# Kernel tuning notes

Hardware: AMD Instinct MI355X
Metric: run time of the kernel (lower is better)

The kernel has to match this reference:

```python
import jax, jax.numpy as jnp
import numpy as np

B, N, M = 2, 16384, 16
D_IN, D_MODEL, D_OUT = 64, 128, 128


def _gather(x, idx):
    # x: (B, N, C), idx: (B, N, M) -> (B, N, M, C)
    return jax.vmap(lambda a, i: a[i])(x, idx)


def setup_inputs() -> dict:
    key = jax.random.key(0)
    ks = jax.random.split(key, 20)

    def w(k, shape, fan_in):
        return (jax.random.normal(k, shape, jnp.float32) / np.sqrt(fan_in)).astype(jnp.float32)

    return {
        "xyz": jax.random.normal(ks[0], (B, N, 3), jnp.float32),
        "feature": jax.random.normal(ks[1], (B, N, D_IN), jnp.float32),
        "neighbors_idx": jax.random.randint(ks[2], (B, N, M), 0, N, jnp.int32),
        # fc_delta: Linear(3, d_model) -> ReLU -> Linear(d_model, d_model)
        "delta_w1": w(ks[3], (3, D_MODEL), 3), "delta_b1": jnp.zeros((D_MODEL,), jnp.float32),
        "delta_w2": w(ks[4], (D_MODEL, D_MODEL), D_MODEL), "delta_b2": jnp.zeros((D_MODEL,), jnp.float32),
        # fc1: Linear(d_in, d_model)
        "fc1_w": w(ks[5], (D_IN, D_MODEL), D_IN), "fc1_b": jnp.zeros((D_MODEL,), jnp.float32),
        # w_qs/w_ks/w_vs: Linear(d_model, d_model, bias=False)
        "wq": w(ks[6], (D_MODEL, D_MODEL), D_MODEL),
        "wk": w(ks[7], (D_MODEL, D_MODEL), D_MODEL),
        "wv": w(ks[8], (D_MODEL, D_MODEL), D_MODEL),
        # fc_gamma: Linear -> ReLU -> Linear
        "gamma_w1": w(ks[9], (D_MODEL, D_MODEL), D_MODEL), "gamma_b1": jnp.zeros((D_MODEL,), jnp.float32),
        "gamma_w2": w(ks[10], (D_MODEL, D_MODEL), D_MODEL), "gamma_b2": jnp.zeros((D_MODEL,), jnp.float32),
        # fc2: Linear(d_model, d_out)
        "fc2_w": w(ks[11], (D_MODEL, D_OUT), D_MODEL), "fc2_b": jnp.zeros((D_OUT,), jnp.float32),
        # shortcut_fc: Linear(d_in, d_out)
        "sc_w": w(ks[12], (D_IN, D_OUT), D_IN), "sc_b": jnp.zeros((D_OUT,), jnp.float32),
    }


def reference(xyz, feature, neighbors_idx,
              delta_w1, delta_b1, delta_w2, delta_b2,
              fc1_w, fc1_b, wq, wk, wv,
              gamma_w1, gamma_b1, gamma_w2, gamma_b2,
              fc2_w, fc2_b, sc_w, sc_b):
    # relative positions of k neighbors: (B, N, M, 3)
    raw = xyz[:, :, None, :] - _gather(xyz, neighbors_idx)
    # fc1 projection
    f = feature @ fc1_w + fc1_b                       # (B, N, Dm)
    knn_f = _gather(f, neighbors_idx)                 # (B, N, M, Dm)
    q = f @ wq                                        # (B, N, Dm)
    k = knn_f @ wk                                    # (B, N, M, Dm)
    v = knn_f @ wv                                    # (B, N, M, Dm)
    # positional MLP
    pos = jax.nn.relu(raw @ delta_w1 + delta_b1) @ delta_w2 + delta_b2
    # vector attention scores per channel
    attn = q[:, :, None, :] - k + pos
    attn = jax.nn.relu(attn @ gamma_w1 + gamma_b1) @ gamma_w2 + gamma_b2
    attn = jax.nn.softmax(attn / np.sqrt(D_MODEL), axis=-2)  # softmax over M
    # weighted sum over neighbors
    out = jnp.einsum('bnmf,bnmf->bnf', attn, v + pos)  # (B, N, Dm)
    out = out @ fc2_w + fc2_b + (feature @ sc_w + sc_b)
    return out
```

## Files before the change

kernel.cpp:

```cpp
#include <hip/hip_runtime.h>

#define BATCH 2
#define NPTS  16384
#define BN    (BATCH * NPTS)
#define DIN   64
#define DM    128
#define NM    16

__global__ __launch_bounds__(256) void k_proj(
    const float* __restrict__ feat,
    const float* __restrict__ fc1_w, const float* __restrict__ fc1_b,
    const float* __restrict__ wq, const float* __restrict__ wk, const float* __restrict__ wv,
    const float* __restrict__ sc_w, const float* __restrict__ sc_b,
    float* __restrict__ qo, float* __restrict__ kfo, float* __restrict__ vfo,
    float* __restrict__ outp)
{
    __shared__ __align__(16) float featb[64][DIN];
    __shared__ __align__(16) float fbuf[64][DM];
    const int tid = threadIdx.x;
    const int p0  = blockIdx.x * 64;

    #pragma unroll
    for (int k = 0; k < 4; ++k) {
        int i4 = tid + k * 256;
        ((float4*)featb)[i4] = ((const float4*)(feat + (size_t)p0 * DIN))[i4];
    }
    __syncthreads();

    const int j    = tid & 127;
    const int base = (tid >> 7) * 32;
    float acc[32];

    #pragma unroll
    for (int pp = 0; pp < 32; ++pp) acc[pp] = fc1_b[j];
    for (int c = 0; c < DIN; c += 4) {
        float w0 = fc1_w[(c + 0) * DM + j];
        float w1 = fc1_w[(c + 1) * DM + j];
        float w2 = fc1_w[(c + 2) * DM + j];
        float w3 = fc1_w[(c + 3) * DM + j];
        #pragma unroll
        for (int pp = 0; pp < 32; ++pp) {
            float4 a = *(const float4*)&featb[base + pp][c];
            acc[pp] += a.x * w0 + a.y * w1 + a.z * w2 + a.w * w3;
        }
    }
    #pragma unroll
    for (int pp = 0; pp < 32; ++pp) fbuf[base + pp][j] = acc[pp];
    __syncthreads();

    for (int pass = 0; pass < 3; ++pass) {
        const float* W = pass == 0 ? wq : (pass == 1 ? wk : wv);
        float*       O = pass == 0 ? qo : (pass == 1 ? kfo : vfo);
        #pragma unroll
        for (int pp = 0; pp < 32; ++pp) acc[pp] = 0.f;
        for (int c = 0; c < DM; c += 4) {
            float w0 = W[(c + 0) * DM + j];
            float w1 = W[(c + 1) * DM + j];
            float w2 = W[(c + 2) * DM + j];
            float w3 = W[(c + 3) * DM + j];
            #pragma unroll
            for (int pp = 0; pp < 32; ++pp) {
                float4 a = *(const float4*)&fbuf[base + pp][c];
                acc[pp] += a.x * w0 + a.y * w1 + a.z * w2 + a.w * w3;
            }
        }
        #pragma unroll
        for (int pp = 0; pp < 32; ++pp) O[(size_t)(p0 + base + pp) * DM + j] = acc[pp];
    }

    #pragma unroll
    for (int pp = 0; pp < 32; ++pp) acc[pp] = sc_b[j];
    for (int c = 0; c < DIN; c += 4) {
        float w0 = sc_w[(c + 0) * DM + j];
        float w1 = sc_w[(c + 1) * DM + j];
        float w2 = sc_w[(c + 2) * DM + j];
        float w3 = sc_w[(c + 3) * DM + j];
        #pragma unroll
        for (int pp = 0; pp < 32; ++pp) {
            float4 a = *(const float4*)&featb[base + pp][c];
            acc[pp] += a.x * w0 + a.y * w1 + a.z * w2 + a.w * w3;
        }
    }
    #pragma unroll
    for (int pp = 0; pp < 32; ++pp) outp[(size_t)(p0 + base + pp) * DM + j] = acc[pp];
}

#define ASW(r) (((r) >> 1) & 3)

#define FMA16(O, W) do { \
    O[0]  += a0.x * (W); O[1]  += a0.y * (W); O[2]  += a0.z * (W); O[3]  += a0.w * (W); \
    O[4]  += a1.x * (W); O[5]  += a1.y * (W); O[6]  += a1.z * (W); O[7]  += a1.w * (W); \
    O[8]  += a2.x * (W); O[9]  += a2.y * (W); O[10] += a2.z * (W); O[11] += a2.w * (W); \
    O[12] += a3.x * (W); O[13] += a3.y * (W); O[14] += a3.z * (W); O[15] += a3.w * (W); } while (0)

__device__ __forceinline__ void mm128(
    const float* __restrict__ Wg,
    float (* __restrict__ wbuf)[DM],
    const float (* __restrict__ aw)[NM],
    float* __restrict__ o0, float* __restrict__ o1,
    int tid, int lane)
{
    for (int c0 = 0; c0 < DM; c0 += 16) {
        __syncthreads();
        #pragma unroll
        for (int k2 = 0; k2 < 2; ++k2) {
            int i4 = tid + k2 * 256;
            ((float4*)wbuf)[i4] = ((const float4*)(Wg + (size_t)c0 * DM))[i4];
        }
        __syncthreads();
        #pragma unroll
        for (int cc = 0; cc < 16; ++cc) {
            const int s = (cc >> 1) & 3;
            float w0 = wbuf[cc][lane];
            float w1 = wbuf[cc][64 + lane];
            const float4* ar = (const float4*)&aw[c0 + cc][0];
            const float4 a0 = ar[0 ^ s];
            const float4 a1 = ar[1 ^ s];
            const float4 a2 = ar[2 ^ s];
            const float4 a3 = ar[3 ^ s];
            FMA16(o0, w0);
            FMA16(o1, w1);
        }
    }
}

__global__ __launch_bounds__(256, 2) void k_attn(
    const float* __restrict__ xyz, const int* __restrict__ nidx,
    const float* __restrict__ qg, const float* __restrict__ kfg, const float* __restrict__ vfg,
    const float* __restrict__ dw1, const float* __restrict__ db1,
    const float* __restrict__ dw2, const float* __restrict__ db2,
    const float* __restrict__ gw1, const float* __restrict__ gb1,
    const float* __restrict__ gw2, const float* __restrict__ gb2,
    float* __restrict__ ao)
{
    __shared__ __align__(16) float abuf[4][DM][NM];
    __shared__ __align__(16) float obuf[4][NM][DM];
    __shared__ __align__(16) float wbuf[16][DM];
    __shared__ __align__(16) float raws[4][NM][4];
    __shared__ int idxs[4][NM];

    const int tid  = threadIdx.x;
    const int wave = tid >> 6;
    const int lane = tid & 63;
    const int p    = blockIdx.x * 4 + wave;
    const int b    = p >> 14;

    if (lane < NM) {
        int jj = nidx[(size_t)p * NM + lane];
        idxs[wave][lane] = jj;
        const float* xc = xyz + (size_t)p * 3;
        const float* xn = xyz + ((size_t)b * NPTS + jj) * 3;
        raws[wave][lane][0] = xc[0] - xn[0];
        raws[wave][lane][1] = xc[1] - xn[1];
        raws[wave][lane][2] = xc[2] - xn[2];
        raws[wave][lane][3] = 0.f;
    }
    const float q0 = qg[(size_t)p * DM + lane];
    const float q1 = qg[(size_t)p * DM + 64 + lane];
    __syncthreads();

    const int sw = ASW(lane);
    float4* arow0 = (float4*)&abuf[wave][lane][0];
    float4* arow1 = (float4*)&abuf[wave][64 + lane][0];

    #pragma unroll 4
    for (int m = 0; m < NM; ++m) {
        int jj = idxs[wave][m];
        size_t r = ((size_t)b * NPTS + jj) * DM;
        obuf[wave][m][lane]      = q0 - kfg[r + lane];
        obuf[wave][m][64 + lane] = q1 - kfg[r + 64 + lane];
    }

    float o0[16], o1[16];

    {
        float wA0 = dw1[lane],          wB0 = dw1[64 + lane];
        float wA1 = dw1[DM + lane],     wB1 = dw1[DM + 64 + lane];
        float wA2 = dw1[2 * DM + lane], wB2 = dw1[2 * DM + 64 + lane];
        float bA = db1[lane], bB = db1[64 + lane];
        #pragma unroll
        for (int m = 0; m < NM; ++m) {
            float4 r4 = *(const float4*)&raws[wave][m][0];
            o0[m] = fmaxf(bA + r4.x * wA0 + r4.y * wA1 + r4.z * wA2, 0.f);
            o1[m] = fmaxf(bB + r4.x * wB0 + r4.y * wB1 + r4.z * wB2, 0.f);
        }
        #pragma unroll
        for (int g = 0; g < 4; ++g) {
            arow0[g ^ sw] = make_float4(o0[4*g+0], o0[4*g+1], o0[4*g+2], o0[4*g+3]);
            arow1[g ^ sw] = make_float4(o1[4*g+0], o1[4*g+1], o1[4*g+2], o1[4*g+3]);
        }
    }

    {
        float bA = db2[lane], bB = db2[64 + lane];
        #pragma unroll
        for (int m = 0; m < NM; ++m) { o0[m] = bA; o1[m] = bB; }
    }
    mm128(dw2, wbuf, abuf[wave], o0, o1, tid, lane);

    #pragma unroll
    for (int g = 0; g < 4; ++g) {
        float4 t0, t1;
        t0.x = obuf[wave][4*g+0][lane] + o0[4*g+0];
        t0.y = obuf[wave][4*g+1][lane] + o0[4*g+1];
        t0.z = obuf[wave][4*g+2][lane] + o0[4*g+2];
        t0.w = obuf[wave][4*g+3][lane] + o0[4*g+3];
        t1.x = obuf[wave][4*g+0][64 + lane] + o1[4*g+0];
        t1.y = obuf[wave][4*g+1][64 + lane] + o1[4*g+1];
        t1.z = obuf[wave][4*g+2][64 + lane] + o1[4*g+2];
        t1.w = obuf[wave][4*g+3][64 + lane] + o1[4*g+3];
        arow0[g ^ sw] = t0;
        arow1[g ^ sw] = t1;
    }
    #pragma unroll 4
    for (int m = 0; m < NM; ++m) {
        int jj = idxs[wave][m];
        size_t r = ((size_t)b * NPTS + jj) * DM;
        obuf[wave][m][lane]      = vfg[r + lane] + o0[m];
        obuf[wave][m][64 + lane] = vfg[r + 64 + lane] + o1[m];
    }

    {
        float bA = gb1[lane], bB = gb1[64 + lane];
        #pragma unroll
        for (int m = 0; m < NM; ++m) { o0[m] = bA; o1[m] = bB; }
    }
    mm128(gw1, wbuf, abuf[wave], o0, o1, tid, lane);
    #pragma unroll
    for (int g = 0; g < 4; ++g) {
        arow0[g ^ sw] = make_float4(fmaxf(o0[4*g+0], 0.f), fmaxf(o0[4*g+1], 0.f),
                                    fmaxf(o0[4*g+2], 0.f), fmaxf(o0[4*g+3], 0.f));
        arow1[g ^ sw] = make_float4(fmaxf(o1[4*g+0], 0.f), fmaxf(o1[4*g+1], 0.f),
                                    fmaxf(o1[4*g+2], 0.f), fmaxf(o1[4*g+3], 0.f));
    }

    {
        float bA = gb2[lane], bB = gb2[64 + lane];
        #pragma unroll
        for (int m = 0; m < NM; ++m) { o0[m] = bA; o1[m] = bB; }
    }
    mm128(gw2, wbuf, abuf[wave], o0, o1, tid, lane);

    const float scale = 0.08838834764831845f;
    float mx0 = -1e30f, mx1 = -1e30f;
    #pragma unroll
    for (int m = 0; m < NM; ++m) {
        o0[m] *= scale; o1[m] *= scale;
        mx0 = fmaxf(mx0, o0[m]); mx1 = fmaxf(mx1, o1[m]);
    }
    float s0 = 0.f, s1 = 0.f, r0 = 0.f, r1 = 0.f;
    #pragma unroll
    for (int m = 0; m < NM; ++m) {
        float e0 = __expf(o0[m] - mx0);
        float e1 = __expf(o1[m] - mx1);
        s0 += e0; s1 += e1;
        r0 += e0 * obuf[wave][m][lane];
        r1 += e1 * obuf[wave][m][64 + lane];
    }
    ao[(size_t)p * DM + lane]      = r0 / s0;
    ao[(size_t)p * DM + 64 + lane] = r1 / s1;
}

__global__ __launch_bounds__(256) void k_final(
    const float* __restrict__ aog,
    const float* __restrict__ fc2_w, const float* __restrict__ fc2_b,
    float* __restrict__ outp)
{
    __shared__ __align__(16) float ab[64][DM];
    const int tid = threadIdx.x;
    const int p0  = blockIdx.x * 64;

    #pragma unroll
    for (int k = 0; k < 8; ++k) {
        int i4 = tid + k * 256;
        ((float4*)ab)[i4] = ((const float4*)(aog + (size_t)p0 * DM))[i4];
    }
    __syncthreads();

    const int j    = tid & 127;
    const int base = (tid >> 7) * 32;
    float acc[32];
    #pragma unroll
    for (int pp = 0; pp < 32; ++pp) acc[pp] = fc2_b[j];
    for (int c = 0; c < DM; c += 4) {
        float w0 = fc2_w[(c + 0) * DM + j];
        float w1 = fc2_w[(c + 1) * DM + j];
        float w2 = fc2_w[(c + 2) * DM + j];
        float w3 = fc2_w[(c + 3) * DM + j];
        #pragma unroll
        for (int pp = 0; pp < 32; ++pp) {
            float4 a = *(const float4*)&ab[base + pp][c];
            acc[pp] += a.x * w0 + a.y * w1 + a.z * w2 + a.w * w3;
        }
    }
    #pragma unroll
    for (int pp = 0; pp < 32; ++pp) {
        size_t o = (size_t)(p0 + base + pp) * DM + j;
        outp[o] += acc[pp];
    }
}

extern "C" void kernel_launch(void* const* d_in, const int* in_sizes, int n_in,
                              void* d_out, int out_size, void* d_ws, size_t ws_size,
                              hipStream_t stream)
{
    const float* xyz     = (const float*)d_in[0];
    const float* feature = (const float*)d_in[1];
    const int*   nidx    = (const int*)d_in[2];
    const float* dw1     = (const float*)d_in[3];
    const float* db1     = (const float*)d_in[4];
    const float* dw2     = (const float*)d_in[5];
    const float* db2     = (const float*)d_in[6];
    const float* fc1_w   = (const float*)d_in[7];
    const float* fc1_b   = (const float*)d_in[8];
    const float* wq      = (const float*)d_in[9];
    const float* wk      = (const float*)d_in[10];
    const float* wv      = (const float*)d_in[11];
    const float* gw1     = (const float*)d_in[12];
    const float* gb1     = (const float*)d_in[13];
    const float* gw2     = (const float*)d_in[14];
    const float* gb2     = (const float*)d_in[15];
    const float* fc2_w   = (const float*)d_in[16];
    const float* fc2_b   = (const float*)d_in[17];
    const float* sc_w    = (const float*)d_in[18];
    const float* sc_b    = (const float*)d_in[19];

    float* ws = (float*)d_ws;
    const size_t SZ = (size_t)BN * DM;
    float* q  = ws;
    float* kf = ws + SZ;
    float* vf = ws + 2 * SZ;
    float* ao = q;
    float* out = (float*)d_out;

    k_proj<<<BN / 64, 256, 0, stream>>>(feature, fc1_w, fc1_b, wq, wk, wv,
                                        sc_w, sc_b, q, kf, vf, out);
    k_attn<<<BN / 4, 256, 0, stream>>>(xyz, nidx, q, kf, vf,
                                       dw1, db1, dw2, db2,
                                       gw1, gb1, gw2, gb2, ao);
    k_final<<<BN / 64, 256, 0, stream>>>(ao, fc2_w, fc2_b, out);
}
```

Before: 1.140 ms.

## Keep gathered K/V in registers and read weights directly from global

The attention kernel drops the shared obuf, wbuf, raws and idxs buffers and every __syncthreads. Neighbor indices, gathered K and V rows, and relative positions are now loaded straight into per-lane registers. Weight rows are read from global or L2 inside the matmul loop instead of being staged cooperatively in shared memory. This removes block-wide barriers and shared traffic, so each wave runs independently. The cost is 64 extra live registers per lane, which may cut occupancy under launch_bounds(256,2), plus repeated global weight loads per wave.

```diff
diff --git a/kernel.cpp b/kernel.cpp
--- a/kernel.cpp
+++ b/kernel.cpp
@@ -93,26 +93,18 @@
     O[8]  += a2.x * (W); O[9]  += a2.y * (W); O[10] += a2.z * (W); O[11] += a2.w * (W); \
     O[12] += a3.x * (W); O[13] += a3.y * (W); O[14] += a3.z * (W); O[15] += a3.w * (W); } while (0)
 
-__device__ __forceinline__ void mm128(
+__device__ __forceinline__ void mm128g(
     const float* __restrict__ Wg,
-    float (* __restrict__ wbuf)[DM],
     const float (* __restrict__ aw)[NM],
     float* __restrict__ o0, float* __restrict__ o1,
-    int tid, int lane)
+    int lane)
 {
     for (int c0 = 0; c0 < DM; c0 += 16) {
-        __syncthreads();
-        #pragma unroll
-        for (int k2 = 0; k2 < 2; ++k2) {
-            int i4 = tid + k2 * 256;
-            ((float4*)wbuf)[i4] = ((const float4*)(Wg + (size_t)c0 * DM))[i4];
-        }
-        __syncthreads();
         #pragma unroll
         for (int cc = 0; cc < 16; ++cc) {
             const int s = (cc >> 1) & 3;
-            float w0 = wbuf[cc][lane];
-            float w1 = wbuf[cc][64 + lane];
+            const float w0 = Wg[(size_t)(c0 + cc) * DM + lane];
+            const float w1 = Wg[(size_t)(c0 + cc) * DM + 64 + lane];
             const float4* ar = (const float4*)&aw[c0 + cc][0];
             const float4 a0 = ar[0 ^ s];
             const float4 a1 = ar[1 ^ s];
@@ -134,55 +126,52 @@
     float* __restrict__ ao)
 {
     __shared__ __align__(16) float abuf[4][DM][NM];
-    __shared__ __align__(16) float obuf[4][NM][DM];
-    __shared__ __align__(16) float wbuf[16][DM];
-    __shared__ __align__(16) float raws[4][NM][4];
-    __shared__ int idxs[4][NM];
 
     const int tid  = threadIdx.x;
     const int wave = tid >> 6;
     const int lane = tid & 63;
     const int p    = blockIdx.x * 4 + wave;
     const int b    = p >> 14;
-
-    if (lane < NM) {
-        int jj = nidx[(size_t)p * NM + lane];
-        idxs[wave][lane] = jj;
-        const float* xc = xyz + (size_t)p * 3;
-        const float* xn = xyz + ((size_t)b * NPTS + jj) * 3;
-        raws[wave][lane][0] = xc[0] - xn[0];
-        raws[wave][lane][1] = xc[1] - xn[1];
-        raws[wave][lane][2] = xc[2] - xn[2];
-        raws[wave][lane][3] = 0.f;
+    const int rowb = b * NPTS;
+
+    int jjv[NM];
+    #pragma unroll
+    for (int m = 0; m < NM; ++m) jjv[m] = nidx[(size_t)p * NM + m];
+
+    float kv0[NM], kv1[NM], vv0[NM], vv1[NM];
+    #pragma unroll
+    for (int m = 0; m < NM; ++m) {
+        size_t r = (size_t)(rowb + jjv[m]) * DM;
+        kv0[m] = kfg[r + lane];
+        kv1[m] = kfg[r + 64 + lane];
+        vv0[m] = vfg[r + lane];
+        vv1[m] = vfg[r + 64 + lane];
     }
     const float q0 = qg[(size_t)p * DM + lane];
     const float q1 = qg[(size_t)p * DM + 64 + lane];
-    __syncthreads();
 
     const int sw = ASW(lane);
     float4* arow0 = (float4*)&abuf[wave][lane][0];
     float4* arow1 = (float4*)&abuf[wave][64 + lane][0];
 
-    #pragma unroll 4
-    for (int m = 0; m < NM; ++m) {
-        int jj = idxs[wave][m];
-        size_t r = ((size_t)b * NPTS + jj) * DM;
-        obuf[wave][m][lane]      = q0 - kfg[r + lane];
-        obuf[wave][m][64 + lane] = q1 - kfg[r + 64 + lane];
-    }
-
-    float o0[16], o1[16];
+    float o0[NM], o1[NM];
 
     {
-        float wA0 = dw1[lane],          wB0 = dw1[64 + lane];
-        float wA1 = dw1[DM + lane],     wB1 = dw1[DM + 64 + lane];
-        float wA2 = dw1[2 * DM + lane], wB2 = dw1[2 * DM + 64 + lane];
-        float bA = db1[lane], bB = db1[64 + lane];
+        const float xc0 = xyz[(size_t)p * 3 + 0];
+        const float xc1 = xyz[(size_t)p * 3 + 1];
+        const float xc2 = xyz[(size_t)p * 3 + 2];
+        const float wA0 = dw1[lane],          wB0 = dw1[64 + lane];
+        const float wA1 = dw1[DM + lane],     wB1 = dw1[DM + 64 + lane];
+        const float wA2 = dw1[2 * DM + lane], wB2 = dw1[2 * DM + 64 + lane];
+        const float bA = db1[lane], bB = db1[64 + lane];
         #pragma unroll
         for (int m = 0; m < NM; ++m) {
-            float4 r4 = *(const float4*)&raws[wave][m][0];
-            o0[m] = fmaxf(bA + r4.x * wA0 + r4.y * wA1 + r4.z * wA2, 0.f);
-            o1[m] = fmaxf(bB + r4.x * wB0 + r4.y * wB1 + r4.z * wB2, 0.f);
+            size_t xr = (size_t)(rowb + jjv[m]) * 3;
+            float r0 = xc0 - xyz[xr + 0];
+            float r1 = xc1 - xyz[xr + 1];
+            float r2 = xc2 - xyz[xr + 2];
+            o0[m] = fmaxf(bA + r0 * wA0 + r1 * wA1 + r2 * wA2, 0.f);
+            o1[m] = fmaxf(bB + r0 * wB0 + r1 * wB1 + r2 * wB2, 0.f);
         }
         #pragma unroll
         for (int g = 0; g < 4; ++g) {
@@ -192,40 +181,31 @@
     }
 
     {
-        float bA = db2[lane], bB = db2[64 + lane];
+        const float bA = db2[lane], bB = db2[64 + lane];
         #pragma unroll
         for (int m = 0; m < NM; ++m) { o0[m] = bA; o1[m] = bB; }
     }
-    mm128(dw2, wbuf, abuf[wave], o0, o1, tid, lane);
-
+    mm128g(dw2, abuf[wave], o0, o1, lane);
+
+    #pragma unroll
+    for (int m = 0; m < NM; ++m) {
+        kv0[m] = (q0 - kv0[m]) + o0[m];
+        kv1[m] = (q1 - kv1[m]) + o1[m];
+        vv0[m] += o0[m];
+        vv1[m] += o1[m];
+    }
     #pragma unroll
     for (int g = 0; g < 4; ++g) {
-        float4 t0, t1;
-        t0.x = obuf[wave][4*g+0][lane] + o0[4*g+0];
-        t0.y = obuf[wave][4*g+1][lane] + o0[4*g+1];
-        t0.z = obuf[wave][4*g+2][lane] + o0[4*g+2];
-        t0.w = obuf[wave][4*g+3][lane] + o0[4*g+3];
-        t1.x = obuf[wave][4*g+0][64 + lane] + o1[4*g+0];
-        t1.y = obuf[wave][4*g+1][64 + lane] + o1[4*g+1];
-        t1.z = obuf[wave][4*g+2][64 + lane] + o1[4*g+2];
-        t1.w = obuf[wave][4*g+3][64 + lane] + o1[4*g+3];
-        arow0[g ^ sw] = t0;
-        arow1[g ^ sw] = t1;
-    }
-    #pragma unroll 4
-    for (int m = 0; m < NM; ++m) {
-        int jj = idxs[wave][m];
-        size_t r = ((size_t)b * NPTS + jj) * DM;
-        obuf[wave][m][lane]      = vfg[r + lane] + o0[m];
-        obuf[wave][m][64 + lane] = vfg[r + 64 + lane] + o1[m];
+        arow0[g ^ sw] = make_float4(kv0[4*g+0], kv0[4*g+1], kv0[4*g+2], kv0[4*g+3]);
+        arow1[g ^ sw] = make_float4(kv1[4*g+0], kv1[4*g+1], kv1[4*g+2], kv1[4*g+3]);
     }
 
     {
-        float bA = gb1[lane], bB = gb1[64 + lane];
+        const float bA = gb1[lane], bB = gb1[64 + lane];
         #pragma unroll
         for (int m = 0; m < NM; ++m) { o0[m] = bA; o1[m] = bB; }
     }
-    mm128(gw1, wbuf, abuf[wave], o0, o1, tid, lane);
+    mm128g(gw1, abuf[wave], o0, o1, lane);
     #pragma unroll
     for (int g = 0; g < 4; ++g) {
         arow0[g ^ sw] = make_float4(fmaxf(o0[4*g+0], 0.f), fmaxf(o0[4*g+1], 0.f),
@@ -235,11 +215,11 @@
     }
 
     {
-        float bA = gb2[lane], bB = gb2[64 + lane];
+        const float bA = gb2[lane], bB = gb2[64 + lane];
         #pragma unroll
         for (int m = 0; m < NM; ++m) { o0[m] = bA; o1[m] = bB; }
     }
-    mm128(gw2, wbuf, abuf[wave], o0, o1, tid, lane);
+    mm128g(gw2, abuf[wave], o0, o1, lane);
 
     const float scale = 0.08838834764831845f;
     float mx0 = -1e30f, mx1 = -1e30f;
@@ -254,8 +234,8 @@
         float e0 = __expf(o0[m] - mx0);
         float e1 = __expf(o1[m] - mx1);
         s0 += e0; s1 += e1;
-        r0 += e0 * obuf[wave][m][lane];
-        r1 += e1 * obuf[wave][m][64 + lane];
+        r0 += e0 * vv0[m];
+        r1 += e1 * vv1[m];
     }
     ao[(size_t)p * DM + lane]      = r0 / s0;
     ao[(size_t)p * DM + 64 + lane] = r1 / s1;
```

New measurement: 1.297 ms. 13.7% more time.
